# Optimization experiments

Measured on AMD Instinct MI355X. Metric: run time of the kernel, lower is better.

Reference implementation:

```python
import jax, jax.numpy as jnp
import numpy as np

NG, ND = 100000, 20000          # gene / disease node counts
F_IN, HID, OUT = 128, 128, 64
E_GG, E_GD, E_DG = 400000, 100000, 100000
SLOPE = 0.2                      # PyG GATConv LeakyReLU default


def setup_inputs() -> dict:
    key = jax.random.key(0)
    ks = jax.random.split(key, 26)
    s1 = 1.0 / np.sqrt(F_IN)
    s2 = 1.0 / np.sqrt(HID)
    inp = {
        "x_gene": jax.random.normal(ks[0], (NG, F_IN), jnp.float32),
        "x_disease": jax.random.normal(ks[1], (ND, F_IN), jnp.float32),
        # layer-1 GAT params, stacked over edge types [g2g, g2d, d2g]
        "Wsrc1": jax.random.normal(ks[2], (3, F_IN, HID), jnp.float32) * s1,
        "Wdst1": jax.random.normal(ks[3], (3, F_IN, HID), jnp.float32) * s1,
        "atts1": jax.random.normal(ks[4], (3, HID), jnp.float32) * s2,
        "attd1": jax.random.normal(ks[5], (3, HID), jnp.float32) * s2,
        "b1": jnp.zeros((3, HID), jnp.float32),
        # layer-2 GAT params
        "Wsrc2": jax.random.normal(ks[6], (3, HID, HID), jnp.float32) * s2,
        "Wdst2": jax.random.normal(ks[7], (3, HID, HID), jnp.float32) * s2,
        "atts2": jax.random.normal(ks[8], (3, HID), jnp.float32) * s2,
        "attd2": jax.random.normal(ks[9], (3, HID), jnp.float32) * s2,
        "b2": jnp.zeros((3, HID), jnp.float32),
        # per-node-type output Linear heads
        "Wg": jax.random.normal(ks[10], (HID, OUT), jnp.float32) * s2,
        "bg": jnp.zeros((OUT,), jnp.float32),
        "Wd": jax.random.normal(ks[11], (HID, OUT), jnp.float32) * s2,
        "bd": jnp.zeros((OUT,), jnp.float32),
        # edge lists (src, dst) per edge type
        "g2g_src": jax.random.randint(ks[12], (E_GG,), 0, NG, jnp.int32),
        "g2g_dst": jax.random.randint(ks[13], (E_GG,), 0, NG, jnp.int32),
        "g2d_src": jax.random.randint(ks[14], (E_GD,), 0, NG, jnp.int32),
        "g2d_dst": jax.random.randint(ks[15], (E_GD,), 0, ND, jnp.int32),
        "d2g_src": jax.random.randint(ks[16], (E_DG,), 0, ND, jnp.int32),
        "d2g_dst": jax.random.randint(ks[17], (E_DG,), 0, NG, jnp.int32),
    }
    return inp


def _gat(x_src, x_dst, src, dst, Ws, Wd, a_s, a_d, b, n_dst):
    """Single-head PyG GATConv (bipartite, add_self_loops=False)."""
    hs = x_src @ Ws                     # [Ns, H] projected source feats
    e_src = hs @ a_s                    # [Ns]
    e_dst = (x_dst @ Wd) @ a_d          # [Nd]
    e = jax.nn.leaky_relu(e_src[src] + e_dst[dst], SLOPE)  # [E]
    # segment softmax over destination nodes
    m = jax.ops.segment_max(e, dst, num_segments=n_dst)    # -inf for empty
    ex = jnp.exp(e - m[dst])
    denom = jax.ops.segment_sum(ex, dst, num_segments=n_dst)
    alpha = ex / denom[dst]             # [E]
    out = jax.ops.segment_sum(alpha[:, None] * hs[src], dst, num_segments=n_dst)
    return out + b


def reference(x_gene, x_disease, Wsrc1, Wdst1, atts1, attd1, b1,
              Wsrc2, Wdst2, atts2, attd2, b2, Wg, bg, Wd, bd,
              g2g_src, g2g_dst, g2d_src, g2d_dst, d2g_src, d2g_dst):
    def layer(xg, xd, Ws, Wdst, a_s, a_d, b):
        # HeteroConv default aggr='sum' over edge types per destination type
        og = (_gat(xg, xg, g2g_src, g2g_dst, Ws[0], Wdst[0], a_s[0], a_d[0], b[0], NG)
              + _gat(xd, xg, d2g_src, d2g_dst, Ws[2], Wdst[2], a_s[2], a_d[2], b[2], NG))
        od = _gat(xg, xd, g2d_src, g2d_dst, Ws[1], Wdst[1], a_s[1], a_d[1], b[1], ND)
        return og, od

    hg, hd = layer(x_gene, x_disease, Wsrc1, Wdst1, atts1, attd1, b1)
    hg, hd = jax.nn.relu(hg), jax.nn.relu(hd)
    hg, hd = layer(hg, hd, Wsrc2, Wdst2, atts2, attd2, b2)
    hg, hd = jax.nn.relu(hg), jax.nn.relu(hd)
    out_gene = hg @ Wg + bg             # [NG, OUT]
    out_disease = hd @ Wd + bd          # [ND, OUT]
    # concatenate per-type outputs (gene first) into one array
    return jnp.concatenate([out_gene, out_disease], axis=0)
```

## Files before the change

### kernel.cpp

```cpp
#include <hip/hip_runtime.h>
#include <hip/hip_bf16.h>
#include <cstdint>
#include <cstddef>

#define NGENE 100000
#define NDIS  20000
#define FDIM  128
#define HIDD  128
#define OUTF  64
#define EGG   400000
#define EGD   100000
#define EDG   100000
#define ETOT  (EGG + EGD + EDG)
#define NSLOT (NGENE + NDIS + NGENE)
#define NSRC  (2 * NGENE + NDIS)
#define SLOPE 0.2f

typedef __attribute__((ext_vector_type(8))) short short8;
typedef __attribute__((ext_vector_type(4))) float f32x4;

static __device__ __forceinline__ float leaky(float x) { return x > 0.f ? x : SLOPE * x; }

static __device__ __forceinline__ ushort f2b(float x) {
    uint u = __float_as_uint(x);
    return (ushort)((u + 0x7fffu + ((u >> 16) & 1u)) >> 16);
}
static __device__ __forceinline__ float b2f(uint s) { return __uint_as_float(s << 16); }
static __device__ __forceinline__ uint pack2(float lo, float hi) {
    return (uint)f2b(lo) | ((uint)f2b(hi) << 16);
}

__global__ __launch_bounds__(256) void conv_f32_bf16(const float* __restrict__ in,
                                                     ushort* __restrict__ out, int n4)
{
    int i = blockIdx.x * 256 + threadIdx.x;
    if (i >= n4) return;
    float4 v = ((const float4*)in)[i];
    ushort4 o; o.x = f2b(v.x); o.y = f2b(v.y); o.z = f2b(v.z); o.w = f2b(v.w);
    ((ushort4*)out)[i] = o;
}

__global__ __launch_bounds__(256) void conv_wt_all(const float* __restrict__ Ws1, const float* __restrict__ Ws2,
                                                   const float* __restrict__ Wg,  const float* __restrict__ Wd,
                                                   ushort* __restrict__ wt1, ushort* __restrict__ wt2,
                                                   ushort* __restrict__ wtg, ushort* __restrict__ wtd)
{
    int i = blockIdx.x * 256 + threadIdx.x;
    if (i < 49152) {
        int t = i >> 14, r = i & 16383; int c = r >> 7, k = r & 127;
        wt1[i] = f2b(Ws1[(size_t)t * 16384 + k * 128 + c]);
    } else if (i < 98304) {
        int j = i - 49152;
        int t = j >> 14, r = j & 16383; int c = r >> 7, k = r & 127;
        wt2[j] = f2b(Ws2[(size_t)t * 16384 + k * 128 + c]);
    } else if (i < 106496) {
        int j = i - 98304; int c = j >> 7, k = j & 127;
        wtg[j] = f2b(Wg[k * 64 + c]);
    } else if (i < 114688) {
        int j = i - 106496; int c = j >> 7, k = j & 127;
        wtd[j] = f2b(Wd[k * 64 + c]);
    }
}

__global__ __launch_bounds__(64) void compute_av(const float* __restrict__ Ws1, const float* __restrict__ Wd1,
                                                 const float* __restrict__ as1, const float* __restrict__ ad1,
                                                 const float* __restrict__ Ws2, const float* __restrict__ Wd2,
                                                 const float* __restrict__ as2, const float* __restrict__ ad2,
                                                 float* __restrict__ av)
{
    int b = blockIdx.x;
    int mat = b >> 7, f = b & 127;
    int layer = mat / 6, idx = mat % 6;
    int t = (idx < 3) ? idx : idx - 3;
    const float* W; const float* a;
    if (layer == 0) { W = (idx < 3) ? Ws1 : Wd1; a = (idx < 3) ? as1 : ad1; }
    else           { W = (idx < 3) ? Ws2 : Wd2; a = (idx < 3) ? as2 : ad2; }
    const float* Wrow = W + ((size_t)t * 128 + f) * 128;
    const float* avec = a + t * 128;
    int lane = threadIdx.x;
    float2 w  = ((const float2*)Wrow)[lane];
    float2 aa = ((const float2*)avec)[lane];
    float d = w.x * aa.x + w.y * aa.y;
    for (int off = 32; off; off >>= 1) d += __shfl_down(d, off);
    if (lane == 0) av[mat * 128 + f] = d;
}

template<int NCOL, int WAVES, int NDOT, bool OUT_BF16>
__global__ __launch_bounds__(WAVES * 64) void gemm_mfma(const ushort* __restrict__ X,
                                                        const ushort* __restrict__ Wt,
                                                        const float* __restrict__ bias,
                                                        void* __restrict__ H, int N,
                                                        const float* __restrict__ av, int4 vidx,
                                                        float* __restrict__ oes,
                                                        float* __restrict__ oda,
                                                        float* __restrict__ odb)
{
    constexpr int NT  = NCOL / (16 * WAVES);
    constexpr int CPW = 16 * NT;
    __shared__ ushort xs[64 * 128];
    const int tid = threadIdx.x;
    const int r0  = blockIdx.x * 64;
    const int w = tid >> 6, l = tid & 63;
    const int lr = l & 15, lk = l >> 4;

    short8 bfrag[NT][4];
    const short8* Wt8 = (const short8*)Wt;
    #pragma unroll
    for (int nt = 0; nt < NT; ++nt)
        #pragma unroll
        for (int ks = 0; ks < 4; ++ks)
            bfrag[nt][ks] = Wt8[(w * CPW + nt * 16 + lr) * 16 + ks * 4 + lk];

    for (int ci = tid; ci < 1024; ci += WAVES * 64) {
        int r = ci >> 4; int bc = (ci & 15) << 4;
        int4 v = make_int4(0, 0, 0, 0);
        if (r0 + r < N) v = *(const int4*)((const char*)X + (size_t)(r0 + r) * 256 + bc);
        *(int4*)((char*)xs + r * 256 + (bc ^ ((r & 7) << 4))) = v;
    }
    __syncthreads();

    f32x4 acc[4][NT];
    #pragma unroll
    for (int rc = 0; rc < 4; ++rc)
        #pragma unroll
        for (int nt = 0; nt < NT; ++nt) acc[rc][nt] = f32x4{0.f, 0.f, 0.f, 0.f};

    #pragma unroll
    for (int rc = 0; rc < 4; ++rc) {
        int ar = rc * 16 + lr;
        #pragma unroll
        for (int ks = 0; ks < 4; ++ks) {
            short8 a = *(const short8*)((const char*)xs + ar * 256 + ((ks * 64 + lk * 16) ^ ((ar & 7) << 4)));
            #pragma unroll
            for (int nt = 0; nt < NT; ++nt)
                acc[rc][nt] = __builtin_amdgcn_mfma_f32_16x16x32_bf16(a, bfrag[nt][ks], acc[rc][nt], 0, 0, 0);
        }
    }

    #pragma unroll
    for (int rc = 0; rc < 4; ++rc) {
        #pragma unroll
        for (int nt = 0; nt < NT; ++nt) {
            int col = w * CPW + nt * 16 + lr;
            float bv = OUT_BF16 ? 0.f : bias[col];
            #pragma unroll
            for (int q = 0; q < 4; ++q) {
                int gr = r0 + rc * 16 + lk * 4 + q;
                if (gr < N) {
                    if (OUT_BF16) ((ushort*)H)[(size_t)gr * NCOL + col] = f2b(acc[rc][nt][q]);
                    else          ((float*)H)[(size_t)gr * NCOL + col] = acc[rc][nt][q] + bv;
                }
            }
        }
    }

    if (NDOT > 0) {
        constexpr int TPR = WAVES;
        constexpr int KCH = 128 / TPR;
        int row = tid / TPR;
        int kq  = tid % TPR;
        int gr  = r0 + row;
        float xv[KCH];
        #pragma unroll
        for (int j = 0; j < KCH / 8; ++j) {
            int bc = kq * (KCH * 2) + j * 16;
            uint4 u = *(const uint4*)((const char*)xs + row * 256 + (bc ^ ((row & 7) << 4)));
            xv[j*8+0] = b2f(u.x & 0xffffu); xv[j*8+1] = b2f(u.x >> 16);
            xv[j*8+2] = b2f(u.y & 0xffffu); xv[j*8+3] = b2f(u.y >> 16);
            xv[j*8+4] = b2f(u.z & 0xffffu); xv[j*8+5] = b2f(u.z >> 16);
            xv[j*8+6] = b2f(u.w & 0xffffu); xv[j*8+7] = b2f(u.w >> 16);
        }
        int vi[4] = { vidx.x, vidx.y, vidx.z, vidx.w };
        float dots[NDOT > 0 ? NDOT : 1];
        #pragma unroll
        for (int v = 0; v < NDOT; ++v) {
            const float* a = av + vi[v] * 128 + kq * KCH;
            float d = 0.f;
            #pragma unroll
            for (int k = 0; k < KCH; ++k) d += xv[k] * a[k];
            #pragma unroll
            for (int off = 1; off < TPR; off <<= 1) d += __shfl_xor(d, off);
            dots[v] = d;
        }
        if (kq == 0 && gr < N) {
            if (NDOT == 4) {
                *(float2*)(oes + 2 * gr) = make_float2(dots[0], dots[1]);
                oda[gr] = dots[2];
                odb[gr] = dots[3];
            } else if (NDOT == 2) {
                oes[gr] = dots[0];
                oda[gr] = dots[1];
            }
        }
    }
}

__global__ void hist_edges(const int* __restrict__ gg_d, const int* __restrict__ gd_d,
                           const int* __restrict__ dg_d, int* __restrict__ counts)
{
    int i = blockIdx.x * blockDim.x + threadIdx.x;
    if (i >= ETOT) return;
    int slot;
    if (i < EGG) slot = gg_d[i];
    else if (i < EGG + EGD) slot = NGENE + gd_d[i - EGG];
    else slot = NGENE + NDIS + dg_d[i - EGG - EGD];
    atomicAdd(&counts[slot], 1);
}

__global__ __launch_bounds__(256) void scan_blocks(const int* __restrict__ counts, int* __restrict__ rowptr,
                                                   int* __restrict__ partials, int n)
{
    __shared__ int sdata[256];
    int base = blockIdx.x * 2048;
    int tid  = threadIdx.x;
    int local[8]; int s = 0;
    #pragma unroll
    for (int j = 0; j < 8; ++j) {
        int idx = base + tid * 8 + j;
        int v = (idx < n) ? counts[idx] : 0;
        local[j] = s; s += v;
    }
    sdata[tid] = s;
    __syncthreads();
    for (int off = 1; off < 256; off <<= 1) {
        int v = 0;
        if (tid >= off) v = sdata[tid - off];
        __syncthreads();
        if (tid >= off) sdata[tid] += v;
        __syncthreads();
    }
    int texcl = (tid ? sdata[tid - 1] : 0);
    #pragma unroll
    for (int j = 0; j < 8; ++j) {
        int idx = base + tid * 8 + j;
        if (idx < n) rowptr[idx] = local[j] + texcl;
    }
    if (tid == 255) partials[blockIdx.x] = sdata[255];
}

__global__ __launch_bounds__(256) void scan_partials(int* __restrict__ partials, int nb)
{
    __shared__ int sdata[256];
    int tid = threadIdx.x;
    sdata[tid] = (tid < nb) ? partials[tid] : 0;
    __syncthreads();
    for (int off = 1; off < 256; off <<= 1) {
        int v = 0;
        if (tid >= off) v = sdata[tid - off];
        __syncthreads();
        if (tid >= off) sdata[tid] += v;
        __syncthreads();
    }
    partials[tid] = (tid ? sdata[tid - 1] : 0);
}

__global__ void scan_add(int* __restrict__ rowptr, const int* __restrict__ partials, int n,
                         int* __restrict__ cursor)
{
    int i = blockIdx.x * blockDim.x + threadIdx.x;
    if (i < n) {
        int v = rowptr[i] + partials[i >> 11];
        rowptr[i] = v;
        cursor[i] = v;
    }
    if (i == 0) rowptr[n] = ETOT;
}

__global__ void scatter_edges(const int* __restrict__ gg_s, const int* __restrict__ gg_d,
                              const int* __restrict__ gd_s, const int* __restrict__ gd_d,
                              const int* __restrict__ dg_s, const int* __restrict__ dg_d,
                              int* __restrict__ cursor, int* __restrict__ colu)
{
    int i = blockIdx.x * blockDim.x + threadIdx.x;
    if (i >= ETOT) return;
    int slot, srcu;
    if (i < EGG) { slot = gg_d[i]; srcu = 2 * gg_s[i]; }
    else if (i < EGG + EGD) { int j = i - EGG; slot = NGENE + gd_d[j]; srcu = 2 * gd_s[j] + 1; }
    else { int j = i - EGG - EGD; slot = NGENE + NDIS + dg_d[j]; srcu = 2 * NGENE + dg_s[j]; }
    int pos = atomicAdd(&cursor[slot], 1);
    colu[pos] = srcu;
}

__device__ __forceinline__ void seg_go(int slot, const int* __restrict__ rowptr,
                                       const int* __restrict__ colu, const float* __restrict__ su,
                                       const float* __restrict__ edu, const uint4* __restrict__ hsu,
                                       int gl, float acc[8])
{
    int s = rowptr[slot], e = rowptr[slot + 1];
    if (e <= s) return;
    float edv = edu[slot];
    float sx[8];
    #pragma unroll
    for (int j = 0; j < 8; ++j) sx[j] = 0.f;
    float den = 0.f;
    int c = colu[s]; float sc = su[c];
    uint4 h = hsu[(size_t)c * 16 + gl];
    for (int i = s + 1; i < e; ++i) {
        int c1 = colu[i]; float sc1 = su[c1];
        uint4 h1 = hsu[(size_t)c1 * 16 + gl];
        float el = sc + edv; el = el > 0.f ? el : SLOPE * el;
        float p = __expf(fminf(el, 80.f));
        den += p;
        sx[0] += p * b2f(h.x & 0xffffu); sx[1] += p * b2f(h.x >> 16);
        sx[2] += p * b2f(h.y & 0xffffu); sx[3] += p * b2f(h.y >> 16);
        sx[4] += p * b2f(h.z & 0xffffu); sx[5] += p * b2f(h.z >> 16);
        sx[6] += p * b2f(h.w & 0xffffu); sx[7] += p * b2f(h.w >> 16);
        sc = sc1; h = h1;
    }
    float el = sc + edv; el = el > 0.f ? el : SLOPE * el;
    float p = __expf(fminf(el, 80.f));
    den += p;
    sx[0] += p * b2f(h.x & 0xffffu); sx[1] += p * b2f(h.x >> 16);
    sx[2] += p * b2f(h.y & 0xffffu); sx[3] += p * b2f(h.y >> 16);
    sx[4] += p * b2f(h.z & 0xffffu); sx[5] += p * b2f(h.z >> 16);
    sx[6] += p * b2f(h.w & 0xffffu); sx[7] += p * b2f(h.w >> 16);
    float inv = 1.0f / den;
    #pragma unroll
    for (int j = 0; j < 8; ++j) acc[j] += sx[j] * inv;
}

template<bool TWO>
__global__ __launch_bounds__(256) void agg_seg(const int* __restrict__ rowptr, const int* __restrict__ colu,
                                              const float* __restrict__ su, const float* __restrict__ edu,
                                              const uint4* __restrict__ hsu,
                                              int slotA0, int slotB0,
                                              const float* __restrict__ biasA, const float* __restrict__ biasB,
                                              uint4* __restrict__ out, int N)
{
    int g  = blockIdx.x * 16 + (threadIdx.x >> 4);
    int gl = threadIdx.x & 15;
    if (g >= N) return;
    float acc[8];
    #pragma unroll
    for (int j = 0; j < 8; ++j) acc[j] = 0.f;
    seg_go(slotA0 + g, rowptr, colu, su, edu, hsu, gl, acc);
    if (TWO) seg_go(slotB0 + g, rowptr, colu, su, edu, hsu, gl, acc);

    float4 bA0 = ((const float4*)biasA)[gl * 2];
    float4 bA1 = ((const float4*)biasA)[gl * 2 + 1];
    float b0 = bA0.x, b1 = bA0.y, b2 = bA0.z, b3 = bA0.w;
    float b4 = bA1.x, b5 = bA1.y, b6 = bA1.z, b7 = bA1.w;
    if (TWO) {
        float4 bB0 = ((const float4*)biasB)[gl * 2];
        float4 bB1 = ((const float4*)biasB)[gl * 2 + 1];
        b0 += bB0.x; b1 += bB0.y; b2 += bB0.z; b3 += bB0.w;
        b4 += bB1.x; b5 += bB1.y; b6 += bB1.z; b7 += bB1.w;
    }
    uint4 o;
    o.x = pack2(fmaxf(acc[0] + b0, 0.f), fmaxf(acc[1] + b1, 0.f));
    o.y = pack2(fmaxf(acc[2] + b2, 0.f), fmaxf(acc[3] + b3, 0.f));
    o.z = pack2(fmaxf(acc[4] + b4, 0.f), fmaxf(acc[5] + b5, 0.f));
    o.w = pack2(fmaxf(acc[6] + b6, 0.f), fmaxf(acc[7] + b7, 0.f));
    out[(size_t)g * 16 + gl] = o;
}

extern "C" void kernel_launch(void* const* d_in, const int* in_sizes, int n_in,
                              void* d_out, int out_size, void* d_ws, size_t ws_size,
                              hipStream_t stream)
{
    const float* xg  = (const float*)d_in[0];
    const float* xd  = (const float*)d_in[1];
    const float* Ws1 = (const float*)d_in[2];
    const float* Wd1 = (const float*)d_in[3];
    const float* as1 = (const float*)d_in[4];
    const float* ad1 = (const float*)d_in[5];
    const float* b1  = (const float*)d_in[6];
    const float* Ws2 = (const float*)d_in[7];
    const float* Wd2 = (const float*)d_in[8];
    const float* as2 = (const float*)d_in[9];
    const float* ad2 = (const float*)d_in[10];
    const float* b2  = (const float*)d_in[11];
    const float* Wg  = (const float*)d_in[12];
    const float* bg  = (const float*)d_in[13];
    const float* Wdh = (const float*)d_in[14];
    const float* bd  = (const float*)d_in[15];
    const int* gg_s = (const int*)d_in[16];
    const int* gg_d = (const int*)d_in[17];
    const int* gd_s = (const int*)d_in[18];
    const int* gd_d = (const int*)d_in[19];
    const int* dg_s = (const int*)d_in[20];
    const int* dg_d = (const int*)d_in[21];
    float* out = (float*)d_out;

    size_t p = 0;
    char* ws = (char*)d_ws;
    auto alloc_f = [&](size_t n) { p = (p + 255) & ~(size_t)255; float* r = (float*)(ws + p);  p += n * sizeof(float);  return r; };
    auto alloc_i = [&](size_t n) { p = (p + 255) & ~(size_t)255; int* r = (int*)(ws + p);      p += n * sizeof(int);    return r; };
    auto alloc_u = [&](size_t n) { p = (p + 255) & ~(size_t)255; ushort* r = (ushort*)(ws + p); p += n * sizeof(ushort); return r; };

    ushort* xgb  = alloc_u((size_t)NGENE * FDIM);
    ushort* xdb  = alloc_u((size_t)NDIS  * FDIM);
    ushort* hsu  = alloc_u((size_t)NSRC * HIDD);
    ushort* h1gb = alloc_u((size_t)NGENE * HIDD);
    ushort* h1db = alloc_u((size_t)NDIS  * HIDD);
    ushort* wt1  = alloc_u(3 * 128 * 128);
    ushort* wt2  = alloc_u(3 * 128 * 128);
    ushort* wtg  = alloc_u(64 * 128);
    ushort* wtd  = alloc_u(64 * 128);
    float* av   = alloc_f(12 * 128);
    float* esu  = alloc_f(NSRC);
    float* edu  = alloc_f(NSLOT);
    int* counts   = alloc_i(NSLOT);
    int* rowptr   = alloc_i(NSLOT + 1);
    int* partials = alloc_i(256);
    int* colu     = alloc_i(ETOT);
    (void)ws_size; (void)in_sizes; (void)n_in; (void)out_size;

    const int SCAN_BLOCKS = (NSLOT + 2047) / 2048;

    ushort* hs_dis = hsu + (size_t)2 * NGENE * HIDD;
    float* es_dis = esu + 2 * NGENE;
    float* ed0 = edu;
    float* ed1 = edu + NGENE;
    float* ed2 = edu + NGENE + NDIS;

    hipMemsetAsync(counts, 0, (size_t)NSLOT * sizeof(int), stream);
    hist_edges<<<(ETOT + 255) / 256, 256, 0, stream>>>(gg_d, gd_d, dg_d, counts);
    scan_blocks<<<SCAN_BLOCKS, 256, 0, stream>>>(counts, rowptr, partials, NSLOT);
    scan_partials<<<1, 256, 0, stream>>>(partials, SCAN_BLOCKS);
    scan_add<<<(NSLOT + 255) / 256, 256, 0, stream>>>(rowptr, partials, NSLOT, counts);
    scatter_edges<<<(ETOT + 255) / 256, 256, 0, stream>>>(gg_s, gg_d, gd_s, gd_d, dg_s, dg_d,
                                                          counts, colu);

    conv_f32_bf16<<<(NGENE * FDIM / 4 + 255) / 256, 256, 0, stream>>>(xg, xgb, NGENE * FDIM / 4);
    conv_f32_bf16<<<(NDIS  * FDIM / 4 + 255) / 256, 256, 0, stream>>>(xd, xdb, NDIS * FDIM / 4);
    conv_wt_all<<<448, 256, 0, stream>>>(Ws1, Ws2, Wg, Wdh, wt1, wt2, wtg, wtd);
    compute_av<<<1536, 64, 0, stream>>>(Ws1, Wd1, as1, ad1, Ws2, Wd2, as2, ad2, av);

    const int GB_G = (NGENE + 63) / 64, GB_D = (NDIS + 63) / 64;
    const int AB_G = (NGENE + 15) / 16, AB_D = (NDIS + 15) / 16;

    gemm_mfma<256, 8, 4, true><<<GB_G, 512, 0, stream>>>(xgb, wt1, nullptr, hsu, NGENE,
        av, make_int4(0, 1, 3, 5), esu, ed0, ed2);
    gemm_mfma<128, 8, 2, true><<<GB_D, 512, 0, stream>>>(xdb, wt1 + 2 * 128 * 128, nullptr, hs_dis, NDIS,
        av, make_int4(2, 4, 0, 0), es_dis, ed1, nullptr);
    agg_seg<true><<<AB_G, 256, 0, stream>>>(rowptr, colu, esu, edu, (const uint4*)hsu,
        0, NGENE + NDIS, b1 + 0 * 128, b1 + 2 * 128, (uint4*)h1gb, NGENE);
    agg_seg<false><<<AB_D, 256, 0, stream>>>(rowptr, colu, esu, edu, (const uint4*)hsu,
        NGENE, 0, b1 + 1 * 128, nullptr, (uint4*)h1db, NDIS);

    gemm_mfma<256, 8, 4, true><<<GB_G, 512, 0, stream>>>(h1gb, wt2, nullptr, hsu, NGENE,
        av, make_int4(6, 7, 9, 11), esu, ed0, ed2);
    gemm_mfma<128, 8, 2, true><<<GB_D, 512, 0, stream>>>(h1db, wt2 + 2 * 128 * 128, nullptr, hs_dis, NDIS,
        av, make_int4(8, 10, 0, 0), es_dis, ed1, nullptr);
    agg_seg<true><<<AB_G, 256, 0, stream>>>(rowptr, colu, esu, edu, (const uint4*)hsu,
        0, NGENE + NDIS, b2 + 0 * 128, b2 + 2 * 128, (uint4*)h1gb, NGENE);
    agg_seg<false><<<AB_D, 256, 0, stream>>>(rowptr, colu, esu, edu, (const uint4*)hsu,
        NGENE, 0, b2 + 1 * 128, nullptr, (uint4*)h1db, NDIS);

    gemm_mfma<64, 4, 0, false><<<GB_G, 256, 0, stream>>>(h1gb, wtg, bg, out, NGENE,
        av, make_int4(0, 0, 0, 0), nullptr, nullptr, nullptr);
    gemm_mfma<64, 4, 0, false><<<GB_D, 256, 0, stream>>>(h1db, wtd, bd, out + (size_t)NGENE * OUTF, NDIS,
        av, make_int4(0, 0, 0, 0), nullptr, nullptr, nullptr);
}
```

Before: 404.5 us.

## Split each aggregation segment across four sub-groups and fuse prep kernels

The edge aggregation kernel now gives each destination node a full 64-lane wavefront: four 16-lane sub-groups each walk every fourth edge and their partial sums and denominators are combined with cross-lane shuffles. The goal is more memory-level parallelism on the gather of source features, since the old version had one 16-lane group walk each segment serially. It also merges the four preprocessing launches (feature casts, weight transposes, attention vectors) into one kernel to cut launch overhead. In exchange, four times as many lanes are launched per node, many of them idle on short segments, and the shuffle reduction adds work.

```diff
diff --git a/kernel.cpp b/kernel.cpp
--- a/kernel.cpp
+++ b/kernel.cpp
@@ -30,59 +30,66 @@
     return (uint)f2b(lo) | ((uint)f2b(hi) << 16);
 }
 
-__global__ __launch_bounds__(256) void conv_f32_bf16(const float* __restrict__ in,
-                                                     ushort* __restrict__ out, int n4)
-{
-    int i = blockIdx.x * 256 + threadIdx.x;
-    if (i >= n4) return;
-    float4 v = ((const float4*)in)[i];
-    ushort4 o; o.x = f2b(v.x); o.y = f2b(v.y); o.z = f2b(v.z); o.w = f2b(v.w);
-    ((ushort4*)out)[i] = o;
-}
-
-__global__ __launch_bounds__(256) void conv_wt_all(const float* __restrict__ Ws1, const float* __restrict__ Ws2,
-                                                   const float* __restrict__ Wg,  const float* __restrict__ Wd,
-                                                   ushort* __restrict__ wt1, ushort* __restrict__ wt2,
-                                                   ushort* __restrict__ wtg, ushort* __restrict__ wtd)
-{
-    int i = blockIdx.x * 256 + threadIdx.x;
-    if (i < 49152) {
-        int t = i >> 14, r = i & 16383; int c = r >> 7, k = r & 127;
-        wt1[i] = f2b(Ws1[(size_t)t * 16384 + k * 128 + c]);
-    } else if (i < 98304) {
-        int j = i - 49152;
-        int t = j >> 14, r = j & 16383; int c = r >> 7, k = r & 127;
-        wt2[j] = f2b(Ws2[(size_t)t * 16384 + k * 128 + c]);
-    } else if (i < 106496) {
-        int j = i - 98304; int c = j >> 7, k = j & 127;
-        wtg[j] = f2b(Wg[k * 64 + c]);
-    } else if (i < 114688) {
-        int j = i - 106496; int c = j >> 7, k = j & 127;
-        wtd[j] = f2b(Wd[k * 64 + c]);
-    }
-}
-
-__global__ __launch_bounds__(64) void compute_av(const float* __restrict__ Ws1, const float* __restrict__ Wd1,
-                                                 const float* __restrict__ as1, const float* __restrict__ ad1,
-                                                 const float* __restrict__ Ws2, const float* __restrict__ Wd2,
-                                                 const float* __restrict__ as2, const float* __restrict__ ad2,
-                                                 float* __restrict__ av)
-{
-    int b = blockIdx.x;
-    int mat = b >> 7, f = b & 127;
-    int layer = mat / 6, idx = mat % 6;
-    int t = (idx < 3) ? idx : idx - 3;
-    const float* W; const float* a;
-    if (layer == 0) { W = (idx < 3) ? Ws1 : Wd1; a = (idx < 3) ? as1 : ad1; }
-    else           { W = (idx < 3) ? Ws2 : Wd2; a = (idx < 3) ? as2 : ad2; }
-    const float* Wrow = W + ((size_t)t * 128 + f) * 128;
-    const float* avec = a + t * 128;
-    int lane = threadIdx.x;
-    float2 w  = ((const float2*)Wrow)[lane];
-    float2 aa = ((const float2*)avec)[lane];
-    float d = w.x * aa.x + w.y * aa.y;
-    for (int off = 32; off; off >>= 1) d += __shfl_down(d, off);
-    if (lane == 0) av[mat * 128 + f] = d;
+#define PB_XG 12500
+#define PB_XD 15000
+#define PB_WT 15448
+#define PB_AV 15832
+__global__ __launch_bounds__(256) void prep_all(
+    const float* __restrict__ xg, ushort* __restrict__ xgb,
+    const float* __restrict__ xd, ushort* __restrict__ xdb,
+    const float* __restrict__ Ws1, const float* __restrict__ Wd1,
+    const float* __restrict__ as1, const float* __restrict__ ad1,
+    const float* __restrict__ Ws2, const float* __restrict__ Wd2,
+    const float* __restrict__ as2, const float* __restrict__ ad2,
+    const float* __restrict__ Wgh, const float* __restrict__ Wdh,
+    ushort* __restrict__ wt1, ushort* __restrict__ wt2,
+    ushort* __restrict__ wtg, ushort* __restrict__ wtd,
+    float* __restrict__ av)
+{
+    int b = blockIdx.x, tid = threadIdx.x;
+    if (b < PB_XG) {
+        int i = b * 256 + tid;
+        float4 v = ((const float4*)xg)[i];
+        ushort4 o; o.x = f2b(v.x); o.y = f2b(v.y); o.z = f2b(v.z); o.w = f2b(v.w);
+        ((ushort4*)xgb)[i] = o;
+    } else if (b < PB_XD) {
+        int i = (b - PB_XG) * 256 + tid;
+        float4 v = ((const float4*)xd)[i];
+        ushort4 o; o.x = f2b(v.x); o.y = f2b(v.y); o.z = f2b(v.z); o.w = f2b(v.w);
+        ((ushort4*)xdb)[i] = o;
+    } else if (b < PB_WT) {
+        int i = (b - PB_XD) * 256 + tid;
+        if (i < 49152) {
+            int t = i >> 14, r = i & 16383; int c = r >> 7, k = r & 127;
+            wt1[i] = f2b(Ws1[(size_t)t * 16384 + k * 128 + c]);
+        } else if (i < 98304) {
+            int j = i - 49152;
+            int t = j >> 14, r = j & 16383; int c = r >> 7, k = r & 127;
+            wt2[j] = f2b(Ws2[(size_t)t * 16384 + k * 128 + c]);
+        } else if (i < 106496) {
+            int j = i - 98304; int c = j >> 7, k = j & 127;
+            wtg[j] = f2b(Wgh[k * 64 + c]);
+        } else {
+            int j = i - 106496; int c = j >> 7, k = j & 127;
+            wtd[j] = f2b(Wdh[k * 64 + c]);
+        }
+    } else {
+        int idx = (b - PB_WT) * 4 + (tid >> 6);
+        int lane = tid & 63;
+        int mat = idx >> 7, f = idx & 127;
+        int layer = mat / 6, im = mat % 6;
+        int t = (im < 3) ? im : im - 3;
+        const float* W; const float* a;
+        if (layer == 0) { W = (im < 3) ? Ws1 : Wd1; a = (im < 3) ? as1 : ad1; }
+        else           { W = (im < 3) ? Ws2 : Wd2; a = (im < 3) ? as2 : ad2; }
+        const float* Wrow = W + ((size_t)t * 128 + f) * 128;
+        const float* avec = a + t * 128;
+        float2 w  = ((const float2*)Wrow)[lane];
+        float2 aa = ((const float2*)avec)[lane];
+        float d = w.x * aa.x + w.y * aa.y;
+        for (int off = 32; off; off >>= 1) d += __shfl_down(d, off);
+        if (lane == 0) av[mat * 128 + f] = d;
+    }
 }
 
 template<int NCOL, int WAVES, int NDOT, bool OUT_BF16>
@@ -281,10 +288,10 @@
     colu[pos] = srcu;
 }
 
-__device__ __forceinline__ void seg_go(int slot, const int* __restrict__ rowptr,
-                                       const int* __restrict__ colu, const float* __restrict__ su,
-                                       const float* __restrict__ edu, const uint4* __restrict__ hsu,
-                                       int gl, float acc[8])
+__device__ __forceinline__ void seg_go4(int slot, const int* __restrict__ rowptr,
+                                        const int* __restrict__ colu, const float* __restrict__ su,
+                                        const float* __restrict__ edu, const uint4* __restrict__ hsu,
+                                        int sg, int gl, float acc[8])
 {
     int s = rowptr[slot], e = rowptr[slot + 1];
     if (e <= s) return;
@@ -293,11 +300,10 @@
     #pragma unroll
     for (int j = 0; j < 8; ++j) sx[j] = 0.f;
     float den = 0.f;
-    int c = colu[s]; float sc = su[c];
-    uint4 h = hsu[(size_t)c * 16 + gl];
-    for (int i = s + 1; i < e; ++i) {
-        int c1 = colu[i]; float sc1 = su[c1];
-        uint4 h1 = hsu[(size_t)c1 * 16 + gl];
+    for (int i = s + sg; i < e; i += 4) {
+        int c = colu[i];
+        float sc = su[c];
+        uint4 h = hsu[(size_t)c * 16 + gl];
         float el = sc + edv; el = el > 0.f ? el : SLOPE * el;
         float p = __expf(fminf(el, 80.f));
         den += p;
@@ -305,15 +311,14 @@
         sx[2] += p * b2f(h.y & 0xffffu); sx[3] += p * b2f(h.y >> 16);
         sx[4] += p * b2f(h.z & 0xffffu); sx[5] += p * b2f(h.z >> 16);
         sx[6] += p * b2f(h.w & 0xffffu); sx[7] += p * b2f(h.w >> 16);
-        sc = sc1; h = h1;
-    }
-    float el = sc + edv; el = el > 0.f ? el : SLOPE * el;
-    float p = __expf(fminf(el, 80.f));
-    den += p;
-    sx[0] += p * b2f(h.x & 0xffffu); sx[1] += p * b2f(h.x >> 16);
-    sx[2] += p * b2f(h.y & 0xffffu); sx[3] += p * b2f(h.y >> 16);
-    sx[4] += p * b2f(h.z & 0xffffu); sx[5] += p * b2f(h.z >> 16);
-    sx[6] += p * b2f(h.w & 0xffffu); sx[7] += p * b2f(h.w >> 16);
+    }
+    den += __shfl_xor(den, 16);
+    den += __shfl_xor(den, 32);
+    #pragma unroll
+    for (int j = 0; j < 8; ++j) {
+        sx[j] += __shfl_xor(sx[j], 16);
+        sx[j] += __shfl_xor(sx[j], 32);
+    }
     float inv = 1.0f / den;
     #pragma unroll
     for (int j = 0; j < 8; ++j) acc[j] += sx[j] * inv;
@@ -327,14 +332,16 @@
                                               const float* __restrict__ biasA, const float* __restrict__ biasB,
                                               uint4* __restrict__ out, int N)
 {
-    int g  = blockIdx.x * 16 + (threadIdx.x >> 4);
-    int gl = threadIdx.x & 15;
+    int g = blockIdx.x * 4 + (threadIdx.x >> 6);
     if (g >= N) return;
+    int l  = threadIdx.x & 63;
+    int sg = l >> 4, gl = l & 15;
     float acc[8];
     #pragma unroll
     for (int j = 0; j < 8; ++j) acc[j] = 0.f;
-    seg_go(slotA0 + g, rowptr, colu, su, edu, hsu, gl, acc);
-    if (TWO) seg_go(slotB0 + g, rowptr, colu, su, edu, hsu, gl, acc);
+    seg_go4(slotA0 + g, rowptr, colu, su, edu, hsu, sg, gl, acc);
+    if (TWO) seg_go4(slotB0 + g, rowptr, colu, su, edu, hsu, sg, gl, acc);
+    if (sg != 0) return;
 
     float4 bA0 = ((const float4*)biasA)[gl * 2];
     float4 bA1 = ((const float4*)biasA)[gl * 2 + 1];
@@ -370,7 +377,7 @@
     const float* as2 = (const float*)d_in[9];
     const float* ad2 = (const float*)d_in[10];
     const float* b2  = (const float*)d_in[11];
-    const float* Wg  = (const float*)d_in[12];
+    const float* Wgh = (const float*)d_in[12];
     const float* bg  = (const float*)d_in[13];
     const float* Wdh = (const float*)d_in[14];
     const float* bd  = (const float*)d_in[15];
@@ -422,13 +429,12 @@
     scatter_edges<<<(ETOT + 255) / 256, 256, 0, stream>>>(gg_s, gg_d, gd_s, gd_d, dg_s, dg_d,
                                                           counts, colu);
 
-    conv_f32_bf16<<<(NGENE * FDIM / 4 + 255) / 256, 256, 0, stream>>>(xg, xgb, NGENE * FDIM / 4);
-    conv_f32_bf16<<<(NDIS  * FDIM / 4 + 255) / 256, 256, 0, stream>>>(xd, xdb, NDIS * FDIM / 4);
-    conv_wt_all<<<448, 256, 0, stream>>>(Ws1, Ws2, Wg, Wdh, wt1, wt2, wtg, wtd);
-    compute_av<<<1536, 64, 0, stream>>>(Ws1, Wd1, as1, ad1, Ws2, Wd2, as2, ad2, av);
+    prep_all<<<PB_AV, 256, 0, stream>>>(xg, xgb, xd, xdb,
+                                        Ws1, Wd1, as1, ad1, Ws2, Wd2, as2, ad2,
+                                        Wgh, Wdh, wt1, wt2, wtg, wtd, av);
 
     const int GB_G = (NGENE + 63) / 64, GB_D = (NDIS + 63) / 64;
-    const int AB_G = (NGENE + 15) / 16, AB_D = (NDIS + 15) / 16;
+    const int AB_G = (NGENE + 3) / 4, AB_D = (NDIS + 3) / 4;
 
     gemm_mfma<256, 8, 4, true><<<GB_G, 512, 0, stream>>>(xgb, wt1, nullptr, hsu, NGENE,
         av, make_int4(0, 1, 3, 5), esu, ed0, ed2);
```

Result: slower. 438.2 us (+8.3%).
